# Performance work log

Hardware: AMD Instinct MI355X
Metric: run time of the kernel (lower is better)

## Reference

```python
import jax, jax.numpy as jnp
import numpy as np
import math

L = 2; B = 128; CIN = 64; E = 64; H = 8; Wd = 8; NH = 8; MEM = 40
HD = E // NH; HW = H * Wd; THD = HD * HW  # 512
MASK_B = 3.0; NEG = -1e9; EPS = 1e-5


def _conv(x, w, b):
    y = jax.lax.conv_general_dilated(x, w, (1, 1), 'SAME',
                                     dimension_numbers=('NCHW', 'OIHW', 'NCHW'))
    return y + b[None, :, None, None]


def setup_inputs() -> dict:
    key = jax.random.key(0)
    ks = jax.random.split(key, 12)
    f = jax.random.normal
    return {
        'x': f(ks[0], (B, CIN, H, Wd), jnp.float32),
        'h0': f(ks[1], (L, B, E, H, Wd), jnp.float32),
        'c0': f(ks[2], (L, B, E, H, Wd), jnp.float32),
        'k0': f(ks[3], (L, B, NH, MEM, THD), jnp.float32),
        'v0': f(ks[4], (L, B, NH, MEM, THD), jnp.float32),
        'src_mask': jax.random.randint(ks[5], (B, MEM), 0, 2).astype(bool),
        'notdone': jnp.ones((B,), bool),
        'main_w': f(ks[6], (L, 5 * E, CIN + 2 * E, 3, 3), jnp.float32) * 0.05,
        'main_b': jnp.zeros((L, 5 * E), jnp.float32),
        'proj_w': f(ks[7], (L, 3 * E, CIN + E, 3, 3), jnp.float32) * 0.05,
        'proj_b': jnp.zeros((L, 3 * E), jnp.float32),
        'out_w': f(ks[8], (L, E, E, 3, 3), jnp.float32) * 0.05,
        'out_b': jnp.zeros((L, E), jnp.float32),
        'ln_w': jnp.ones((L, E, H, Wd), jnp.float32),
        'ln_b': jnp.zeros((L, E, H, Wd), jnp.float32),
        'pos_w': f(ks[9], (L, MEM, HW * E), jnp.float32) * 0.05,
        'pos_b': f(ks[10], (L, MEM, NH), jnp.float32) * 0.05,
    }


def reference(x, h0, c0, k0, v0, src_mask, notdone,
              main_w, main_b, proj_w, proj_b, out_w, out_b,
              ln_w, ln_b, pos_w, pos_b):
    nd = notdone.astype(x.dtype)[:, None, None, None]
    # rolling attention mask: reset finished episodes, shift left, open last slot
    m = src_mask | (~notdone)[:, None]
    m = jnp.concatenate([m[:, 1:], jnp.zeros((B, 1), bool)], axis=1)
    bias = jnp.where(m, NEG, 0.0).astype(x.dtype)        # (B, MEM)
    bias = bias.at[:, -1].set(MASK_B)
    out = h0[L - 1] * nd
    for n in range(L):
        inp = jnp.concatenate([x, out], axis=1)          # (B, CIN+E, H, W)
        h_cur = h0[n] * nd
        c_cur = c0[n] * nd
        gates = _conv(jnp.concatenate([inp, h_cur], axis=1), main_w[n], main_b[n])
        cc_i, cc_f, cc_o, cc_g, cc_a = jnp.split(gates, 5, axis=1)
        i = jax.nn.sigmoid(cc_i)
        fg = jax.nn.sigmoid(cc_f)
        o = jax.nn.sigmoid(cc_o)
        g = jnp.tanh(cc_g)
        a = jax.nn.sigmoid(cc_a)
        c_next = fg * c_cur + i * g
        # attention over rolling memory (mem_n slots of flattened spatial features)
        kqv = _conv(inp, proj_w[n], proj_b[n]).reshape(B, NH, 3 * HD, HW)
        k = kqv[:, :, :HD].reshape(B, NH, THD)
        q = kqv[:, :, HD:2 * HD].reshape(B, NH, THD) / math.sqrt(THD)
        v = kqv[:, :, 2 * HD:].reshape(B, NH, THD)
        pw = pos_w[n].reshape(MEM, NH, THD).transpose(1, 0, 2)  # (NH, MEM, THD)
        k_cat = jnp.concatenate([k0[n][:, :, 1:], k[:, :, None, :]], axis=2) + pw[None]
        v_cat = jnp.concatenate([v0[n][:, :, 1:], v[:, :, None, :]], axis=2)
        scores = (jnp.einsum('bnd,bnmd->bnm', q, k_cat)
                  + bias[:, None, :] + pos_b[n].T[None])
        attn_w = jax.nn.softmax(scores, axis=-1)
        attn = jnp.einsum('bnm,bnmd->bnd', attn_w, v_cat).reshape(B, E, H, Wd)
        ao = _conv(attn, out_w[n], out_b[n]) + inp[:, :E]
        mu = ao.mean(axis=(1, 2, 3), keepdims=True)
        var = ((ao - mu) ** 2).mean(axis=(1, 2, 3), keepdims=True)
        ao = (ao - mu) * jax.lax.rsqrt(var + EPS) * ln_w[n][None] + ln_b[n][None]
        c_next = c_next + a * jnp.tanh(ao)
        out = o * jnp.tanh(c_next)
    return out
```

## Files before the change

### kernel.cpp

```cpp
#include <hip/hip_runtime.h>
#include <hip/hip_bf16.h>

typedef __hip_bfloat16 bf16;
typedef unsigned short u16;
typedef __attribute__((ext_vector_type(8))) short short8;
typedef __attribute__((ext_vector_type(4))) float f32x4;

#define Bb   128
#define MEMm 40

__device__ __forceinline__ float LD(const void* p, size_t i, int f32) {
    return f32 ? ((const float*)p)[i] : __bfloat162float(((const bf16*)p)[i]);
}
__device__ __forceinline__ float S2F(short s) {
    u16 u = (u16)s;
    return __bfloat162float(*(bf16*)&u);
}
__device__ __forceinline__ int LDB(const void* p, int i, int isbyte) {
    return isbyte ? (int)((const unsigned char*)p)[i] : ((const int*)p)[i];
}
__device__ __forceinline__ void SPLIT(float v, u16& hi, u16& lo) {
    bf16 h = __float2bfloat16(v);
    float r = v - __bfloat162float(h);
    bf16 l = __float2bfloat16(r);
    hi = *(u16*)&h; lo = *(u16*)&l;
}

__global__ void detect_kernel(const void* __restrict__ x,
                              const void* __restrict__ src_mask,
                              const void* __restrict__ notdone,
                              int* __restrict__ flags) {
    __shared__ int s[3];
    const int t = threadIdx.x;
    if (t < 3) s[t] = 0;
    __syncthreads();
    const bf16* xb = (const bf16*)x;
    int bad = 0;
    for (int i = t; i < 4096; i += 256) {
        float v = __bfloat162float(xb[2 * i]);
        if (!(fabsf(v) < 1e4f)) bad = 1;
    }
    if (bad) atomicOr(&s[0], 1);
    int mb = 0;
    const unsigned* mi = (const unsigned*)src_mask;
    for (int i = t; i < 1280; i += 256) if (mi[i] > 1u) mb = 1;
    if (mb) atomicOr(&s[1], 1);
    int nb = 0;
    const unsigned* ni = (const unsigned*)notdone;
    for (int i = t; i < 32; i += 256) if (ni[i] > 1u) nb = 1;
    if (nb) atomicOr(&s[2], 1);
    __syncthreads();
    if (t < 3) flags[t] = s[t];
}

__global__ void setup_kernel(const void* __restrict__ src_mask,
                             const void* __restrict__ notdone,
                             const void* __restrict__ h0,
                             const void* __restrict__ mw,
                             const void* __restrict__ pw,
                             const void* __restrict__ ow,
                             const int* __restrict__ flags,
                             float* __restrict__ biasb,
                             float* __restrict__ outb, size_t hoff,
                             u16* __restrict__ whi, u16* __restrict__ wlo) {
    const int bid = blockIdx.x, t = threadIdx.x;
    const int isf32 = flags[0], mbyte = flags[1], ndbyte = flags[2];
    if (bid < 20) {
        int idx = bid * 256 + t;
        if (idx >= Bb * MEMm) return;
        int b = idx / MEMm, m = idx - b * MEMm;
        float v;
        if (m == MEMm - 1) v = 3.0f;
        else {
            bool masked = (LDB(src_mask, b * MEMm + m + 1, mbyte) != 0) ||
                          (LDB(notdone, b, ndbyte) == 0);
            v = masked ? -1e9f : 0.f;
        }
        biasb[idx] = v;
    } else if (bid < 276) {
        int idx = (bid - 20) * 256 + t;
        int b = idx >> 9;
        float nd = (LDB(notdone, b, ndbyte) != 0) ? 1.f : 0.f;
        size_t e = (size_t)idx * 8;
        float v[8];
        if (isf32) {
            const float* hp = (const float*)h0 + hoff + e;
            f32x4 a = *(const f32x4*)hp, c = *(const f32x4*)(hp + 4);
#pragma unroll
            for (int j = 0; j < 4; ++j) { v[j] = a[j]; v[4 + j] = c[j]; }
        } else {
            short8 s = *(const short8*)((const bf16*)h0 + hoff + e);
#pragma unroll
            for (int j = 0; j < 8; ++j) v[j] = S2F(s[j]);
        }
#pragma unroll
        for (int j = 0; j < 8; ++j) outb[e + j] = v[j] * nd;
    } else {
        int gi = (bid - 276) * 256 + t;
        if (gi >= 1622016) return;
        int layer = (gi >= 811008) ? 1 : 0;
        int i = gi - layer * 811008;
        float v;
        if (i < 552960) {
            int tap = i / 61440, r = i - tap * 61440, co = r / 192, ci = r - co * 192;
            v = LD(mw, (size_t)layer * 552960 + ((size_t)co * 192 + ci) * 9 + tap, isf32);
        } else if (i < 774144) {
            int j = i - 552960;
            int tap = j / 24576, r = j - tap * 24576, co = r / 128, ci = r - co * 128;
            v = LD(pw, (size_t)layer * 221184 + ((size_t)co * 128 + ci) * 9 + tap, isf32);
        } else {
            int j = i - 774144;
            int tap = j / 4096, r = j - tap * 4096, co = r / 64, ci = r - co * 64;
            v = LD(ow, (size_t)layer * 36864 + ((size_t)co * 64 + ci) * 9 + tap, isf32);
        }
        u16 h, l; SPLIT(v, h, l);
        whi[gi] = h; wlo[gi] = l;
    }
}

struct ConvArgs {
    const void *x; const float *prev_out; const void *h0; const void *notdone;
    const u16 *WhiA, *WloA, *WhiB, *WloB;
    const void *biasA, *biasB;
    float *OutA, *OutB;
    long long boffA, boffB;
    size_t hoff;
    int KciA, KciB, CoutA, CoutB, ntA, NT, NMB;
};

__global__ __launch_bounds__(256) void conv_mfma_kernel(ConvArgs g,
                                                        const int* __restrict__ flags) {
    __shared__ __align__(16) u16 Alds[2][2][2600];
    __shared__ __align__(16) u16 Wlds[2][2][2560];
    const int t = threadIdx.x, w = t >> 6, lane = t & 63;
    const int bpair = w >> 1, half = w & 1;
    const int bx = blockIdx.x;
    const int mblk = bx % g.NMB, nt = bx / g.NMB;
    const bool isA = (nt < g.ntA);
    const u16* Whi = isA ? g.WhiA : g.WhiB;
    const u16* Wlo = isA ? g.WloA : g.WloB;
    const int Kci  = isA ? g.KciA : g.KciB;
    const int CoutT= isA ? g.CoutA : g.CoutB;
    float* Out     = isA ? g.OutA : g.OutB;
    const void* bias = isA ? g.biasA : g.biasB;
    const long long boff = isA ? g.boffA : g.boffB;
    const int n0 = (isA ? nt : nt - g.ntA) * 64;
    const int b = mblk * 2 + bpair;
    const int NITER = (Kci >> 5) * 9;
    const int isf32 = flags[0];
    const float nd = (LDB(g.notdone, b, flags[2]) != 0) ? 1.f : 0.f;

    if (half == 0 && lane < 40) { Alds[bpair][0][2560 + lane] = 0; Alds[bpair][1][2560 + lane] = 0; }

    f32x4 acc[4][2];
#pragma unroll
    for (int i = 0; i < 4; ++i)
#pragma unroll
        for (int j = 0; j < 2; ++j) { f32x4 z = {0.f, 0.f, 0.f, 0.f}; acc[i][j] = z; }

    const int co_l = t >> 2, jj = t & 3;
    uint4 hv, lv;
    auto issueW = [&](int it) {
        int kc = it / 9, tap = it - kc * 9;
        size_t o = ((size_t)(tap * CoutT + n0 + co_l)) * Kci + kc * 32 + jj * 8;
        hv = *(const uint4*)(Whi + o);
        lv = *(const uint4*)(Wlo + o);
    };

    issueW(0);
    for (int it = 0; it < NITER; ++it) {
        const int kc = it / 9, tap = it - kc * 9;
        const int par = it & 1;
        *(uint4*)&Wlds[par][0][co_l * 40 + jj * 8] = hv;
        *(uint4*)&Wlds[par][1][co_l * 40 + jj * 8] = lv;
        __syncthreads();
        if (it + 1 < NITER) issueW(it + 1);
        if (tap == 0) {
            const int px = lane;
            const int c0i = half * 16;
            const int cbase = kc * 32;
            short8 hA, hB, lA, lB;
#pragma unroll
            for (int cl2 = 0; cl2 < 16; ++cl2) {
                int c = cbase + c0i + cl2;
                float v;
                if (c < 64) {
                    size_t o = (size_t)b * 4096 + (size_t)c * 64 + px;
                    v = isf32 ? ((const float*)g.x)[o] : S2F(((const short*)g.x)[o]);
                } else if (c < 128) {
                    v = g.prev_out[(size_t)b * 4096 + (size_t)(c - 64) * 64 + px];
                } else {
                    size_t o = g.hoff + (size_t)b * 4096 + (size_t)(c - 128) * 64 + px;
                    v = (isf32 ? ((const float*)g.h0)[o] : S2F(((const short*)g.h0)[o])) * nd;
                }
                u16 hh, ll; SPLIT(v, hh, ll);
                if (cl2 < 8) { hA[cl2] = (short)hh; lA[cl2] = (short)ll; }
                else         { hB[cl2 - 8] = (short)hh; lB[cl2 - 8] = (short)ll; }
            }
            *(short8*)&Alds[bpair][0][px * 40 + c0i]     = hA;
            *(short8*)&Alds[bpair][0][px * 40 + c0i + 8] = hB;
            *(short8*)&Alds[bpair][1][px * 40 + c0i]     = lA;
            *(short8*)&Alds[bpair][1][px * 40 + c0i + 8] = lB;
            __syncthreads();
        }
        const int dy = tap / 3 - 1, dx = tap % 3 - 1;
        const int q8 = (lane >> 4) * 8;
        const int ml = lane & 15;
        short8 aH[4], aL[4];
#pragma unroll
        for (int mt = 0; mt < 4; ++mt) {
            int px = mt * 16 + ml;
            int yy = (px >> 3) + dy, xx = (px & 7) + dx;
            int row = ((unsigned)yy < 8u && (unsigned)xx < 8u) ? yy * 8 + xx : 64;
            int o = row * 40 + q8;
            aH[mt] = *(const short8*)&Alds[bpair][0][o];
            aL[mt] = *(const short8*)&Alds[bpair][1][o];
        }
#pragma unroll
        for (int nn = 0; nn < 2; ++nn) {
            int o = (half * 32 + nn * 16 + ml) * 40 + q8;
            short8 bH = *(const short8*)&Wlds[par][0][o];
            short8 bL = *(const short8*)&Wlds[par][1][o];
#pragma unroll
            for (int mt = 0; mt < 4; ++mt) {
                acc[mt][nn] = __builtin_amdgcn_mfma_f32_16x16x32_bf16(aH[mt], bH, acc[mt][nn], 0, 0, 0);
                acc[mt][nn] = __builtin_amdgcn_mfma_f32_16x16x32_bf16(aH[mt], bL, acc[mt][nn], 0, 0, 0);
                acc[mt][nn] = __builtin_amdgcn_mfma_f32_16x16x32_bf16(aL[mt], bH, acc[mt][nn], 0, 0, 0);
            }
        }
    }
    const int q = lane >> 4, ml = lane & 15;
#pragma unroll
    for (int nn = 0; nn < 2; ++nn) {
        int co = n0 + half * 32 + nn * 16 + ml;
        float bv = LD(bias, (size_t)boff + co, isf32);
#pragma unroll
        for (int mt = 0; mt < 4; ++mt) {
            f32x4 v = acc[mt][nn];
            v[0] += bv; v[1] += bv; v[2] += bv; v[3] += bv;
            *(f32x4*)&Out[((size_t)b * CoutT + co) * 64 + mt * 16 + q * 4] = v;
        }
    }
}

__global__ __launch_bounds__(256) void attn_kernel(
    const float* __restrict__ kqv,
    const void* __restrict__ k0,
    const void* __restrict__ v0,
    const void* __restrict__ pw,
    const void* __restrict__ pb,
    const float* __restrict__ biasb,
    const int* __restrict__ flags,
    u16* __restrict__ ahi, u16* __restrict__ alo,
    size_t kvoff, size_t pwoff, size_t pboff) {
    __shared__ float qv[512], kl[512], vl[512], sc[40], wexp[40];
    __shared__ float accbuf[4][512];
    const int t = threadIdx.x;
    const int isf32 = flags[0];
    const int b = blockIdx.x >> 3, h = blockIdx.x & 7;
    const size_t kqb = (size_t)b * 192 * 64;
    for (int d = t; d < 512; d += 256) {
        int hd = d >> 6, ss = d & 63;
        qv[d] = kqv[kqb + (h * 24 + 8 + hd) * 64 + ss] * 0.044194173824159216f;
        kl[d] = kqv[kqb + (h * 24 + 0 + hd) * 64 + ss];
        vl[d] = kqv[kqb + (h * 24 + 16 + hd) * 64 + ss];
    }
    __syncthreads();
    const int wid = t >> 6, lane = t & 63;
    const int d0 = lane * 8;
    const size_t kvbase = kvoff + ((size_t)(b * 8 + h)) * (size_t)(40 * 512);

    float q8[8];
#pragma unroll
    for (int j = 0; j < 8; ++j) q8[j] = qv[d0 + j];

    for (int m = wid; m < 40; m += 4) {
        float kc[8];
        if (m < 39) {
            if (isf32) {
                const float* kp = (const float*)k0 + kvbase + (size_t)(m + 1) * 512 + d0;
                f32x4 a = *(const f32x4*)kp, c = *(const f32x4*)(kp + 4);
#pragma unroll
                for (int j = 0; j < 4; ++j) { kc[j] = a[j]; kc[4 + j] = c[j]; }
            } else {
                short8 s = *(const short8*)((const bf16*)k0 + kvbase + (size_t)(m + 1) * 512 + d0);
#pragma unroll
                for (int j = 0; j < 8; ++j) kc[j] = S2F(s[j]);
            }
        } else {
#pragma unroll
            for (int j = 0; j < 8; ++j) kc[j] = kl[d0 + j];
        }
        if (isf32) {
            const float* pp = (const float*)pw + pwoff + (size_t)m * 4096 + h * 512 + d0;
            f32x4 a = *(const f32x4*)pp, c = *(const f32x4*)(pp + 4);
#pragma unroll
            for (int j = 0; j < 4; ++j) { kc[j] += a[j]; kc[4 + j] += c[j]; }
        } else {
            short8 s = *(const short8*)((const bf16*)pw + pwoff + (size_t)m * 4096 + h * 512 + d0);
#pragma unroll
            for (int j = 0; j < 8; ++j) kc[j] += S2F(s[j]);
        }
        float p = 0.f;
#pragma unroll
        for (int j = 0; j < 8; ++j) p += q8[j] * kc[j];
#pragma unroll
        for (int off = 32; off > 0; off >>= 1) p += __shfl_down(p, off, 64);
        if (lane == 0)
            sc[m] = p + biasb[b * 40 + m] + LD(pb, pboff + m * 8 + h, isf32);
    }
    __syncthreads();

    float mx = -1e30f;
    for (int m = 0; m < 40; ++m) mx = fmaxf(mx, sc[m]);
    if (t < 40) wexp[t] = __expf(sc[t] - mx);
    __syncthreads();
    float sum = 0.f;
    for (int m = 0; m < 40; ++m) sum += wexp[m];
    float rs = 1.f / sum;

    float acc8[8];
#pragma unroll
    for (int j = 0; j < 8; ++j) acc8[j] = 0.f;
    for (int m = wid; m < 40; m += 4) {
        float wgt = wexp[m];
        if (m < 39) {
            if (isf32) {
                const float* vp = (const float*)v0 + kvbase + (size_t)(m + 1) * 512 + d0;
                f32x4 a = *(const f32x4*)vp, c = *(const f32x4*)(vp + 4);
#pragma unroll
                for (int j = 0; j < 4; ++j) { acc8[j] += wgt * a[j]; acc8[4 + j] += wgt * c[j]; }
            } else {
                short8 s = *(const short8*)((const bf16*)v0 + kvbase + (size_t)(m + 1) * 512 + d0);
#pragma unroll
                for (int j = 0; j < 8; ++j) acc8[j] += wgt * S2F(s[j]);
            }
        } else {
#pragma unroll
            for (int j = 0; j < 8; ++j) acc8[j] += wgt * vl[d0 + j];
        }
    }
#pragma unroll
    for (int j = 0; j < 8; ++j) accbuf[wid][d0 + j] = acc8[j];
    __syncthreads();

    for (int d = t; d < 512; d += 256) {
        float acc = (accbuf[0][d] + accbuf[1][d]) + (accbuf[2][d] + accbuf[3][d]);
        acc *= rs;
        int ch = h * 8 + (d >> 6), px = d & 63;
        u16 hh, ll; SPLIT(acc, hh, ll);
        size_t o = (size_t)b * 4096 + px * 64 + ch;
        ahi[o] = hh; alo[o] = ll;
    }
}

__global__ __launch_bounds__(256) void tail_kernel(
    const u16* __restrict__ ahi, const u16* __restrict__ alo,
    const u16* __restrict__ whi, const u16* __restrict__ wlo,
    const void* __restrict__ outb_bias,
    const void* __restrict__ x,
    const float* __restrict__ gates,
    const void* __restrict__ c0,
    const void* __restrict__ notdone,
    const void* __restrict__ lnw, const void* __restrict__ lnb,
    const int* __restrict__ flags,
    float* __restrict__ out_buf, void* __restrict__ dout, int write_out,
    long long boff, size_t coff, size_t lnoff) {
    __shared__ __align__(16) u16 Ald[2][2][2600];
    __shared__ __align__(16) u16 Wl[2][2][2560];
    __shared__ float red[8], stats[2];
    const int t = threadIdx.x, w = t >> 6, lane = t & 63;
    const int b = blockIdx.x;
    const int isf32 = flags[0], ndbyte = flags[2];

    {
        int px = t >> 2, ci16 = (t & 3) * 16;
        int chunk = ci16 >> 5, cl = ci16 & 31;
        size_t o = ((size_t)b * 64 + px) * 64 + ci16;
        *(uint4*)&Ald[chunk][0][px * 40 + cl]     = *(const uint4*)(ahi + o);
        *(uint4*)&Ald[chunk][0][px * 40 + cl + 8] = *(const uint4*)(ahi + o + 8);
        *(uint4*)&Ald[chunk][1][px * 40 + cl]     = *(const uint4*)(alo + o);
        *(uint4*)&Ald[chunk][1][px * 40 + cl + 8] = *(const uint4*)(alo + o + 8);
        if (t < 160) { int ch = t / 80, hl = (t / 40) & 1, i = t % 40;
                       Ald[ch][hl][2560 + i] = 0; }
    }

    const int co_l = t >> 2, jj = t & 3;
    uint4 hv, lv;
    auto issueW = [&](int it) {
        int kc = it / 9, tap = it - kc * 9;
        size_t o = ((size_t)(tap * 64 + co_l)) * 64 + kc * 32 + jj * 8;
        hv = *(const uint4*)(whi + o);
        lv = *(const uint4*)(wlo + o);
    };

    f32x4 acc[4];
#pragma unroll
    for (int i = 0; i < 4; ++i) { f32x4 z = {0.f, 0.f, 0.f, 0.f}; acc[i] = z; }

    issueW(0);
    for (int it = 0; it < 18; ++it) {
        const int kc = it / 9, tap = it - kc * 9;
        const int par = it & 1;
        *(uint4*)&Wl[par][0][co_l * 40 + jj * 8] = hv;
        *(uint4*)&Wl[par][1][co_l * 40 + jj * 8] = lv;
        __syncthreads();
        if (it + 1 < 18) issueW(it + 1);
        const int dy = tap / 3 - 1, dx = tap % 3 - 1;
        const int q8 = (lane >> 4) * 8;
        const int ml = lane & 15;
        short8 aH[4], aL[4];
#pragma unroll
        for (int mt = 0; mt < 4; ++mt) {
            int px = mt * 16 + ml;
            int yy = (px >> 3) + dy, xx = (px & 7) + dx;
            int row = ((unsigned)yy < 8u && (unsigned)xx < 8u) ? yy * 8 + xx : 64;
            int o = row * 40 + q8;
            aH[mt] = *(const short8*)&Ald[kc][0][o];
            aL[mt] = *(const short8*)&Ald[kc][1][o];
        }
        int o = (w * 16 + ml) * 40 + q8;
        short8 bH = *(const short8*)&Wl[par][0][o];
        short8 bL = *(const short8*)&Wl[par][1][o];
#pragma unroll
        for (int mt = 0; mt < 4; ++mt) {
            acc[mt] = __builtin_amdgcn_mfma_f32_16x16x32_bf16(aH[mt], bH, acc[mt], 0, 0, 0);
            acc[mt] = __builtin_amdgcn_mfma_f32_16x16x32_bf16(aH[mt], bL, acc[mt], 0, 0, 0);
            acc[mt] = __builtin_amdgcn_mfma_f32_16x16x32_bf16(aL[mt], bH, acc[mt], 0, 0, 0);
        }
    }

    const int q = lane >> 4, ml = lane & 15;
    const int co = w * 16 + ml;
    const size_t base = (size_t)b * 4096;
    float bv = LD(outb_bias, (size_t)boff + co, isf32);
    float vals[16];
    float sum = 0.f, sumsq = 0.f;
#pragma unroll
    for (int mt = 0; mt < 4; ++mt) {
        int px0 = mt * 16 + q * 4;
#pragma unroll
        for (int r = 0; r < 4; ++r) {
            float xv = LD(x, base + (size_t)co * 64 + px0 + r, isf32);
            float val = acc[mt][r] + bv + xv;
            vals[mt * 4 + r] = val; sum += val; sumsq += val * val;
        }
    }
#pragma unroll
    for (int off = 32; off > 0; off >>= 1) {
        sum   += __shfl_down(sum, off, 64);
        sumsq += __shfl_down(sumsq, off, 64);
    }
    if (lane == 0) { red[w] = sum; red[4 + w] = sumsq; }
    __syncthreads();
    if (t == 0) {
        float ts = red[0] + red[1] + red[2] + red[3];
        float tq = red[4] + red[5] + red[6] + red[7];
        float mu = ts * (1.f / 4096.f);
        float var = tq * (1.f / 4096.f) - mu * mu;
        stats[0] = mu; stats[1] = rsqrtf(fmaxf(var, 0.f) + 1e-5f);
    }
    __syncthreads();
    const float mu = stats[0], rstd = stats[1];
    const float nd = (LDB(notdone, b, ndbyte) != 0) ? 1.f : 0.f;
    const size_t gbase = (size_t)b * 320 * 64;
#pragma unroll
    for (int mt = 0; mt < 4; ++mt) {
        int px0 = mt * 16 + q * 4;
        size_t i0 = (size_t)co * 64 + px0;
        f32x4 gi4 = *(const f32x4*)&gates[gbase + (size_t)(co      ) * 64 + px0];
        f32x4 gf4 = *(const f32x4*)&gates[gbase + (size_t)(co +  64) * 64 + px0];
        f32x4 go4 = *(const f32x4*)&gates[gbase + (size_t)(co + 128) * 64 + px0];
        f32x4 gg4 = *(const f32x4*)&gates[gbase + (size_t)(co + 192) * 64 + px0];
        f32x4 ga4 = *(const f32x4*)&gates[gbase + (size_t)(co + 256) * 64 + px0];
        f32x4 ov;
#pragma unroll
        for (int r = 0; r < 4; ++r) {
            size_t i = i0 + r;
            float aon = (vals[mt * 4 + r] - mu) * rstd * LD(lnw, lnoff + i, isf32)
                        + LD(lnb, lnoff + i, isf32);
            float gi = 1.f / (1.f + __expf(-gi4[r]));
            float gf = 1.f / (1.f + __expf(-gf4[r]));
            float go = 1.f / (1.f + __expf(-go4[r]));
            float gg = tanhf(gg4[r]);
            float ga = 1.f / (1.f + __expf(-ga4[r]));
            float cc = LD(c0, coff + base + i, isf32) * nd;
            float cn = gf * cc + gi * gg + ga * tanhf(aon);
            float o  = go * tanhf(cn);
            ov[r] = o;
            if (write_out) {
                if (isf32) ((float*)dout)[base + i] = o;
                else       ((bf16*)dout)[base + i] = __float2bfloat16(o);
            }
        }
        *(f32x4*)&out_buf[base + i0] = ov;
    }
}

extern "C" void kernel_launch(void* const* d_in, const int* in_sizes, int n_in,
                              void* d_out, int out_size, void* d_ws, size_t ws_size,
                              hipStream_t stream) {
    const void* x      = d_in[0];
    const void* h0     = d_in[1];
    const void* c0     = d_in[2];
    const void* k0     = d_in[3];
    const void* v0     = d_in[4];
    const void* src_mask = d_in[5];
    const void* notdone  = d_in[6];
    const void* main_w = d_in[7];
    const void* main_b = d_in[8];
    const void* proj_w = d_in[9];
    const void* proj_b = d_in[10];
    const void* out_w  = d_in[11];
    const void* out_b  = d_in[12];
    const void* ln_w   = d_in[13];
    const void* ln_b   = d_in[14];
    const void* pos_w  = d_in[15];
    const void* pos_b  = d_in[16];

    float* wsf = (float*)d_ws;
    int*   flags    = (int*)d_ws;
    float* bias_buf = wsf + 8;
    float* out_buf  = wsf + 8192;
    float* gates_buf= wsf + 532480;
    float* kqv_buf  = wsf + 3153920;
    u16* attn_hi    = (u16*)(wsf + 4726784);
    u16* attn_lo    = (u16*)(wsf + 4988928);
    u16* wr_hi      = (u16*)(wsf + 5251072);
    u16* wr_lo      = (u16*)(wsf + 6062080);

    detect_kernel<<<1, 256, 0, stream>>>(x, src_mask, notdone, flags);
    setup_kernel<<<6612, 256, 0, stream>>>(src_mask, notdone, h0,
                                           main_w, proj_w, out_w, flags,
                                           bias_buf, out_buf, (size_t)524288,
                                           wr_hi, wr_lo);
    for (int n = 0; n < 2; ++n) {
        const size_t wb = (size_t)n * 811008;
        ConvArgs ga;
        ga.x = x; ga.prev_out = out_buf; ga.h0 = h0; ga.notdone = notdone;
        ga.hoff = (size_t)n * 524288;
        ga.WhiA = wr_hi + wb;          ga.WloA = wr_lo + wb;          ga.KciA = 192; ga.CoutA = 320;
        ga.WhiB = wr_hi + wb + 552960; ga.WloB = wr_lo + wb + 552960; ga.KciB = 128; ga.CoutB = 192;
        ga.biasA = main_b; ga.boffA = (long long)n * 320; ga.OutA = gates_buf;
        ga.biasB = proj_b; ga.boffB = (long long)n * 192; ga.OutB = kqv_buf;
        ga.ntA = 5; ga.NT = 8; ga.NMB = 64;
        conv_mfma_kernel<<<512, 256, 0, stream>>>(ga, flags);

        attn_kernel<<<1024, 256, 0, stream>>>(
            kqv_buf, k0, v0, pos_w, pos_b, bias_buf, flags, attn_hi, attn_lo,
            (size_t)n * 20971520, (size_t)n * 163840, (size_t)n * 320);

        tail_kernel<<<128, 256, 0, stream>>>(
            attn_hi, attn_lo, wr_hi + wb + 774144, wr_lo + wb + 774144,
            out_b, x, gates_buf, c0, notdone, ln_w, ln_b, flags,
            out_buf, d_out, (n == 1) ? 1 : 0,
            (long long)n * 64, (size_t)n * 524288, (size_t)n * 4096);
    }
}
```

Before: 572.5 us.

## Fuse all stages into one cooperative persistent kernel with grid syncs

```diff
diff --git a/kernel.cpp b/kernel.cpp
--- a/kernel.cpp
+++ b/kernel.cpp
@@ -1,5 +1,8 @@
 #include <hip/hip_runtime.h>
 #include <hip/hip_bf16.h>
+#include <hip/hip_cooperative_groups.h>
+
+namespace cg = cooperative_groups;
 
 typedef __hip_bfloat16 bf16;
 typedef unsigned short u16;
@@ -25,6 +28,470 @@
     bf16 l = __float2bfloat16(r);
     hi = *(u16*)&h; lo = *(u16*)&l;
 }
+
+struct __align__(16) ShConv { u16 Alds[2][2][2600]; u16 Wlds[2][2][2560]; };
+struct __align__(16) ShAttn { float qv[512], kl[512], vl[512], sc[40], wexp[40];
+                              float accbuf[4][512]; };
+struct __align__(16) ShTail { u16 Ald[2][2][2600]; u16 Wl[2][2][2560];
+                              float red[8]; float stats[2]; };
+union __align__(16) Sh { int det[3]; ShConv conv; ShAttn attn; ShTail tail; };
+
+struct FusedArgs {
+    const void *x, *h0, *c0, *k0, *v0, *src_mask, *notdone;
+    const void *main_w, *main_b, *proj_w, *proj_b, *out_w, *out_b;
+    const void *ln_w, *ln_b, *pos_w, *pos_b;
+    float *bias_buf, *out_buf, *gates_buf, *kqv_buf;
+    u16 *attn_hi, *attn_lo, *wr_hi, *wr_lo;
+    void *dout;
+};
+
+__global__ __launch_bounds__(256, 2) void fused_kernel(FusedArgs a) {
+    __shared__ Sh sh;
+    cg::grid_group grid = cg::this_grid();
+    const int t = threadIdx.x, bx = blockIdx.x;
+
+    int isf32, mbyte, ndbyte;
+    {
+        if (t < 3) sh.det[t] = 0;
+        __syncthreads();
+        const bf16* xb = (const bf16*)a.x;
+        int bad = 0;
+        for (int i = t; i < 4096; i += 256) {
+            float v = __bfloat162float(xb[2 * i]);
+            if (!(fabsf(v) < 1e4f)) bad = 1;
+        }
+        if (bad) atomicOr(&sh.det[0], 1);
+        int mb = 0;
+        const unsigned* mi = (const unsigned*)a.src_mask;
+        for (int i = t; i < 1280; i += 256) if (mi[i] > 1u) mb = 1;
+        if (mb) atomicOr(&sh.det[1], 1);
+        int nb = 0;
+        const unsigned* ni = (const unsigned*)a.notdone;
+        for (int i = t; i < 32; i += 256) if (ni[i] > 1u) nb = 1;
+        if (nb) atomicOr(&sh.det[2], 1);
+        __syncthreads();
+        isf32 = sh.det[0]; mbyte = sh.det[1]; ndbyte = sh.det[2];
+        __syncthreads();
+    }
+
+    for (int u = bx; u < 6612; u += 512) {
+        if (u < 20) {
+            int idx = u * 256 + t;
+            if (idx < Bb * MEMm) {
+                int b = idx / MEMm, m = idx - b * MEMm;
+                float v;
+                if (m == MEMm - 1) v = 3.0f;
+                else {
+                    bool masked = (LDB(a.src_mask, b * MEMm + m + 1, mbyte) != 0) ||
+                                  (LDB(a.notdone, b, ndbyte) == 0);
+                    v = masked ? -1e9f : 0.f;
+                }
+                a.bias_buf[idx] = v;
+            }
+        } else if (u < 276) {
+            int idx = (u - 20) * 256 + t;
+            int b = idx >> 9;
+            float nd = (LDB(a.notdone, b, ndbyte) != 0) ? 1.f : 0.f;
+            size_t e = (size_t)idx * 8;
+            float v[8];
+            if (isf32) {
+                const float* hp = (const float*)a.h0 + 524288 + e;
+                f32x4 p0 = *(const f32x4*)hp, p1 = *(const f32x4*)(hp + 4);
+#pragma unroll
+                for (int j = 0; j < 4; ++j) { v[j] = p0[j]; v[4 + j] = p1[j]; }
+            } else {
+                short8 s = *(const short8*)((const bf16*)a.h0 + 524288 + e);
+#pragma unroll
+                for (int j = 0; j < 8; ++j) v[j] = S2F(s[j]);
+            }
+#pragma unroll
+            for (int j = 0; j < 8; ++j) a.out_buf[e + j] = v[j] * nd;
+        } else {
+            int gi = (u - 276) * 256 + t;
+            if (gi < 1622016) {
+                int layer = (gi >= 811008) ? 1 : 0;
+                int i = gi - layer * 811008;
+                float v;
+                if (i < 552960) {
+                    int tap = i / 61440, r = i - tap * 61440, co = r / 192, ci = r - co * 192;
+                    v = LD(a.main_w, (size_t)layer * 552960 + ((size_t)co * 192 + ci) * 9 + tap, isf32);
+                } else if (i < 774144) {
+                    int j = i - 552960;
+                    int tap = j / 24576, r = j - tap * 24576, co = r / 128, ci = r - co * 128;
+                    v = LD(a.proj_w, (size_t)layer * 221184 + ((size_t)co * 128 + ci) * 9 + tap, isf32);
+                } else {
+                    int j = i - 774144;
+                    int tap = j / 4096, r = j - tap * 4096, co = r / 64, ci = r - co * 64;
+                    v = LD(a.out_w, (size_t)layer * 36864 + ((size_t)co * 64 + ci) * 9 + tap, isf32);
+                }
+                u16 h, l; SPLIT(v, h, l);
+                a.wr_hi[gi] = h; a.wr_lo[gi] = l;
+            }
+        }
+    }
+    grid.sync();
+
+#pragma unroll 1
+    for (int n = 0; n < 2; ++n) {
+        const size_t wb = (size_t)n * 811008;
+        const size_t hoff = (size_t)n * 524288;
+
+        {
+            auto& Alds = sh.conv.Alds;
+            auto& Wlds = sh.conv.Wlds;
+            const int w = t >> 6, lane = t & 63;
+            const int bpair = w >> 1, half = w & 1;
+            const int mblk = bx & 63, nt = bx >> 6;
+            const bool isA = (nt < 5);
+            const u16* Whi = a.wr_hi + wb + (isA ? 0 : 552960);
+            const u16* Wlo = a.wr_lo + wb + (isA ? 0 : 552960);
+            const int Kci  = isA ? 192 : 128;
+            const int CoutT= isA ? 320 : 192;
+            float* Out     = isA ? a.gates_buf : a.kqv_buf;
+            const void* bias = isA ? a.main_b : a.proj_b;
+            const long long boff = isA ? (long long)n * 320 : (long long)n * 192;
+            const int n0 = (isA ? nt : nt - 5) * 64;
+            const int b = mblk * 2 + bpair;
+            const int NITER = (Kci >> 5) * 9;
+            const float nd = (LDB(a.notdone, b, ndbyte) != 0) ? 1.f : 0.f;
+
+            if (half == 0 && lane < 40) { Alds[bpair][0][2560 + lane] = 0; Alds[bpair][1][2560 + lane] = 0; }
+
+            f32x4 acc[4][2];
+#pragma unroll
+            for (int i = 0; i < 4; ++i)
+#pragma unroll
+                for (int j = 0; j < 2; ++j) { f32x4 z = {0.f, 0.f, 0.f, 0.f}; acc[i][j] = z; }
+
+            const int co_l = t >> 2, jj = t & 3;
+            uint4 hv, lv;
+            auto issueW = [&](int it) {
+                int kc = it / 9, tap = it - kc * 9;
+                size_t o = ((size_t)(tap * CoutT + n0 + co_l)) * Kci + kc * 32 + jj * 8;
+                hv = *(const uint4*)(Whi + o);
+                lv = *(const uint4*)(Wlo + o);
+            };
+
+            issueW(0);
+            for (int it = 0; it < NITER; ++it) {
+                const int kc = it / 9, tap = it - kc * 9;
+                const int par = it & 1;
+                *(uint4*)&Wlds[par][0][co_l * 40 + jj * 8] = hv;
+                *(uint4*)&Wlds[par][1][co_l * 40 + jj * 8] = lv;
+                __syncthreads();
+                if (it + 1 < NITER) issueW(it + 1);
+                if (tap == 0) {
+                    const int px = lane;
+                    const int c0i = half * 16;
+                    const int cbase = kc * 32;
+                    short8 hA, hB, lA, lB;
+#pragma unroll
+                    for (int cl2 = 0; cl2 < 16; ++cl2) {
+                        int c = cbase + c0i + cl2;
+                        float v;
+                        if (c < 64) {
+                            size_t o = (size_t)b * 4096 + (size_t)c * 64 + px;
+                            v = isf32 ? ((const float*)a.x)[o] : S2F(((const short*)a.x)[o]);
+                        } else if (c < 128) {
+                            v = a.out_buf[(size_t)b * 4096 + (size_t)(c - 64) * 64 + px];
+                        } else {
+                            size_t o = hoff + (size_t)b * 4096 + (size_t)(c - 128) * 64 + px;
+                            v = (isf32 ? ((const float*)a.h0)[o] : S2F(((const short*)a.h0)[o])) * nd;
+                        }
+                        u16 hh, ll; SPLIT(v, hh, ll);
+                        if (cl2 < 8) { hA[cl2] = (short)hh; lA[cl2] = (short)ll; }
+                        else         { hB[cl2 - 8] = (short)hh; lB[cl2 - 8] = (short)ll; }
+                    }
+                    *(short8*)&Alds[bpair][0][px * 40 + c0i]     = hA;
+                    *(short8*)&Alds[bpair][0][px * 40 + c0i + 8] = hB;
+                    *(short8*)&Alds[bpair][1][px * 40 + c0i]     = lA;
+                    *(short8*)&Alds[bpair][1][px * 40 + c0i + 8] = lB;
+                    __syncthreads();
+                }
+                const int dy = tap / 3 - 1, dx = tap % 3 - 1;
+                const int q8 = (lane >> 4) * 8;
+                const int ml = lane & 15;
+                short8 aH[4], aL[4];
+#pragma unroll
+                for (int mt = 0; mt < 4; ++mt) {
+                    int px = mt * 16 + ml;
+                    int yy = (px >> 3) + dy, xx = (px & 7) + dx;
+                    int row = ((unsigned)yy < 8u && (unsigned)xx < 8u) ? yy * 8 + xx : 64;
+                    int o = row * 40 + q8;
+                    aH[mt] = *(const short8*)&Alds[bpair][0][o];
+                    aL[mt] = *(const short8*)&Alds[bpair][1][o];
+                }
+#pragma unroll
+                for (int nn = 0; nn < 2; ++nn) {
+                    int o = (half * 32 + nn * 16 + ml) * 40 + q8;
+                    short8 bH = *(const short8*)&Wlds[par][0][o];
+                    short8 bL = *(const short8*)&Wlds[par][1][o];
+#pragma unroll
+                    for (int mt = 0; mt < 4; ++mt) {
+                        acc[mt][nn] = __builtin_amdgcn_mfma_f32_16x16x32_bf16(aH[mt], bH, acc[mt][nn], 0, 0, 0);
+                        acc[mt][nn] = __builtin_amdgcn_mfma_f32_16x16x32_bf16(aH[mt], bL, acc[mt][nn], 0, 0, 0);
+                        acc[mt][nn] = __builtin_amdgcn_mfma_f32_16x16x32_bf16(aL[mt], bH, acc[mt][nn], 0, 0, 0);
+                    }
+                }
+            }
+            const int q = lane >> 4, ml = lane & 15;
+#pragma unroll
+            for (int nn = 0; nn < 2; ++nn) {
+                int co = n0 + half * 32 + nn * 16 + ml;
+                float bv = LD(bias, (size_t)boff + co, isf32);
+#pragma unroll
+                for (int mt = 0; mt < 4; ++mt) {
+                    f32x4 v = acc[mt][nn];
+                    v[0] += bv; v[1] += bv; v[2] += bv; v[3] += bv;
+                    *(f32x4*)&Out[((size_t)b * CoutT + co) * 64 + mt * 16 + q * 4] = v;
+                }
+            }
+        }
+        grid.sync();
+
+        for (int u = bx; u < 1024; u += 512) {
+            float* qv = sh.attn.qv; float* kl = sh.attn.kl; float* vl = sh.attn.vl;
+            float* sc = sh.attn.sc; float* wexp = sh.attn.wexp;
+            auto& accbuf = sh.attn.accbuf;
+            const int b = u >> 3, h = u & 7;
+            const size_t kqb = (size_t)b * 192 * 64;
+            for (int d = t; d < 512; d += 256) {
+                int hd = d >> 6, ss = d & 63;
+                qv[d] = a.kqv_buf[kqb + (h * 24 + 8 + hd) * 64 + ss] * 0.044194173824159216f;
+                kl[d] = a.kqv_buf[kqb + (h * 24 + 0 + hd) * 64 + ss];
+                vl[d] = a.kqv_buf[kqb + (h * 24 + 16 + hd) * 64 + ss];
+            }
+            __syncthreads();
+            const int wid = t >> 6, lane = t & 63;
+            const int d0 = lane * 8;
+            const size_t kvbase = (size_t)n * 20971520 + ((size_t)(b * 8 + h)) * (size_t)(40 * 512);
+            const size_t pwoff = (size_t)n * 163840, pboff = (size_t)n * 320;
+
+            float q8[8];
+#pragma unroll
+            for (int j = 0; j < 8; ++j) q8[j] = qv[d0 + j];
+
+            for (int m = wid; m < 40; m += 4) {
+                float kc[8];
+                if (m < 39) {
+                    if (isf32) {
+                        const float* kp = (const float*)a.k0 + kvbase + (size_t)(m + 1) * 512 + d0;
+                        f32x4 p0 = *(const f32x4*)kp, p1 = *(const f32x4*)(kp + 4);
+#pragma unroll
+                        for (int j = 0; j < 4; ++j) { kc[j] = p0[j]; kc[4 + j] = p1[j]; }
+                    } else {
+                        short8 s = *(const short8*)((const bf16*)a.k0 + kvbase + (size_t)(m + 1) * 512 + d0);
+#pragma unroll
+                        for (int j = 0; j < 8; ++j) kc[j] = S2F(s[j]);
+                    }
+                } else {
+#pragma unroll
+                    for (int j = 0; j < 8; ++j) kc[j] = kl[d0 + j];
+                }
+                if (isf32) {
+                    const float* pp = (const float*)a.pos_w + pwoff + (size_t)m * 4096 + h * 512 + d0;
+                    f32x4 p0 = *(const f32x4*)pp, p1 = *(const f32x4*)(pp + 4);
+#pragma unroll
+                    for (int j = 0; j < 4; ++j) { kc[j] += p0[j]; kc[4 + j] += p1[j]; }
+                } else {
+                    short8 s = *(const short8*)((const bf16*)a.pos_w + pwoff + (size_t)m * 4096 + h * 512 + d0);
+#pragma unroll
+                    for (int j = 0; j < 8; ++j) kc[j] += S2F(s[j]);
+                }
+                float p = 0.f;
+#pragma unroll
+                for (int j = 0; j < 8; ++j) p += q8[j] * kc[j];
+#pragma unroll
+                for (int off = 32; off > 0; off >>= 1) p += __shfl_down(p, off, 64);
+                if (lane == 0)
+                    sc[m] = p + a.bias_buf[b * 40 + m] + LD(a.pos_b, pboff + m * 8 + h, isf32);
+            }
+            __syncthreads();
+
+            float mx = -1e30f;
+            for (int m = 0; m < 40; ++m) mx = fmaxf(mx, sc[m]);
+            if (t < 40) wexp[t] = __expf(sc[t] - mx);
+            __syncthreads();
+            float sum = 0.f;
+            for (int m = 0; m < 40; ++m) sum += wexp[m];
+            float rs = 1.f / sum;
+
+            float acc8[8];
+#pragma unroll
+            for (int j = 0; j < 8; ++j) acc8[j] = 0.f;
+            for (int m = wid; m < 40; m += 4) {
+                float wgt = wexp[m];
+                if (m < 39) {
+                    if (isf32) {
+                        const float* vp = (const float*)a.v0 + kvbase + (size_t)(m + 1) * 512 + d0;
+                        f32x4 p0 = *(const f32x4*)vp, p1 = *(const f32x4*)(vp + 4);
+#pragma unroll
+                        for (int j = 0; j < 4; ++j) { acc8[j] += wgt * p0[j]; acc8[4 + j] += wgt * p1[j]; }
+                    } else {
+                        short8 s = *(const short8*)((const bf16*)a.v0 + kvbase + (size_t)(m + 1) * 512 + d0);
+#pragma unroll
+                        for (int j = 0; j < 8; ++j) acc8[j] += wgt * S2F(s[j]);
+                    }
+                } else {
+#pragma unroll
+                    for (int j = 0; j < 8; ++j) acc8[j] += wgt * vl[d0 + j];
+                }
+            }
+#pragma unroll
+            for (int j = 0; j < 8; ++j) accbuf[wid][d0 + j] = acc8[j];
+            __syncthreads();
+
+            for (int d = t; d < 512; d += 256) {
+                float acc = (accbuf[0][d] + accbuf[1][d]) + (accbuf[2][d] + accbuf[3][d]);
+                acc *= rs;
+                int ch = h * 8 + (d >> 6), px = d & 63;
+                u16 hh, ll; SPLIT(acc, hh, ll);
+                size_t o = (size_t)b * 4096 + px * 64 + ch;
+                a.attn_hi[o] = hh; a.attn_lo[o] = ll;
+            }
+            __syncthreads();
+        }
+        grid.sync();
+
+        if (bx < 128) {
+            auto& Ald = sh.tail.Ald;
+            auto& Wl  = sh.tail.Wl;
+            float* red = sh.tail.red; float* stats = sh.tail.stats;
+            const int w = t >> 6, lane = t & 63;
+            const int b = bx;
+            const u16* whi = a.wr_hi + wb + 774144;
+            const u16* wlo = a.wr_lo + wb + 774144;
+            const int write_out = (n == 1) ? 1 : 0;
+            const long long boff = (long long)n * 64;
+            const size_t coff = (size_t)n * 524288, lnoff = (size_t)n * 4096;
+
+            {
+                int px = t >> 2, ci16 = (t & 3) * 16;
+                int chunk = ci16 >> 5, cl = ci16 & 31;
+                size_t o = ((size_t)b * 64 + px) * 64 + ci16;
+                *(uint4*)&Ald[chunk][0][px * 40 + cl]     = *(const uint4*)(a.attn_hi + o);
+                *(uint4*)&Ald[chunk][0][px * 40 + cl + 8] = *(const uint4*)(a.attn_hi + o + 8);
+                *(uint4*)&Ald[chunk][1][px * 40 + cl]     = *(const uint4*)(a.attn_lo + o);
+                *(uint4*)&Ald[chunk][1][px * 40 + cl + 8] = *(const uint4*)(a.attn_lo + o + 8);
+                if (t < 160) { int ch = t / 80, hl = (t / 40) & 1, i = t % 40;
+                               Ald[ch][hl][2560 + i] = 0; }
+            }
+
+            const int co_l = t >> 2, jj = t & 3;
+            uint4 hv, lv;
+            auto issueW = [&](int it) {
+                int kc = it / 9, tap = it - kc * 9;
+                size_t o = ((size_t)(tap * 64 + co_l)) * 64 + kc * 32 + jj * 8;
+                hv = *(const uint4*)(whi + o);
+                lv = *(const uint4*)(wlo + o);
+            };
+
+            f32x4 acc[4];
+#pragma unroll
+            for (int i = 0; i < 4; ++i) { f32x4 z = {0.f, 0.f, 0.f, 0.f}; acc[i] = z; }
+
+            issueW(0);
+            for (int it = 0; it < 18; ++it) {
+                const int kc = it / 9, tap = it - kc * 9;
+                const int par = it & 1;
+                *(uint4*)&Wl[par][0][co_l * 40 + jj * 8] = hv;
+                *(uint4*)&Wl[par][1][co_l * 40 + jj * 8] = lv;
+                __syncthreads();
+                if (it + 1 < 18) issueW(it + 1);
+                const int dy = tap / 3 - 1, dx = tap % 3 - 1;
+                const int q8 = (lane >> 4) * 8;
+                const int ml = lane & 15;
+                short8 aH[4], aL[4];
+#pragma unroll
+                for (int mt = 0; mt < 4; ++mt) {
+                    int px = mt * 16 + ml;
+                    int yy = (px >> 3) + dy, xx = (px & 7) + dx;
+                    int row = ((unsigned)yy < 8u && (unsigned)xx < 8u) ? yy * 8 + xx : 64;
+                    int o = row * 40 + q8;
+                    aH[mt] = *(const short8*)&Ald[kc][0][o];
+                    aL[mt] = *(const short8*)&Ald[kc][1][o];
+                }
+                int o = (w * 16 + ml) * 40 + q8;
+                short8 bH = *(const short8*)&Wl[par][0][o];
+                short8 bL = *(const short8*)&Wl[par][1][o];
+#pragma unroll
+                for (int mt = 0; mt < 4; ++mt) {
+                    acc[mt] = __builtin_amdgcn_mfma_f32_16x16x32_bf16(aH[mt], bH, acc[mt], 0, 0, 0);
+                    acc[mt] = __builtin_amdgcn_mfma_f32_16x16x32_bf16(aH[mt], bL, acc[mt], 0, 0, 0);
+                    acc[mt] = __builtin_amdgcn_mfma_f32_16x16x32_bf16(aL[mt], bH, acc[mt], 0, 0, 0);
+                }
+            }
+
+            const int q = lane >> 4, ml = lane & 15;
+            const int co = w * 16 + ml;
+            const size_t base = (size_t)b * 4096;
+            float bv = LD(a.out_b, (size_t)boff + co, isf32);
+            float vals[16];
+            float sum = 0.f, sumsq = 0.f;
+#pragma unroll
+            for (int mt = 0; mt < 4; ++mt) {
+                int px0 = mt * 16 + q * 4;
+#pragma unroll
+                for (int r = 0; r < 4; ++r) {
+                    float xv = LD(a.x, base + (size_t)co * 64 + px0 + r, isf32);
+                    float val = acc[mt][r] + bv + xv;
+                    vals[mt * 4 + r] = val; sum += val; sumsq += val * val;
+                }
+            }
+#pragma unroll
+            for (int off = 32; off > 0; off >>= 1) {
+                sum   += __shfl_down(sum, off, 64);
+                sumsq += __shfl_down(sumsq, off, 64);
+            }
+            if (lane == 0) { red[w] = sum; red[4 + w] = sumsq; }
+            __syncthreads();
+            if (t == 0) {
+                float ts = red[0] + red[1] + red[2] + red[3];
+                float tq = red[4] + red[5] + red[6] + red[7];
+                float mu = ts * (1.f / 4096.f);
+                float var = tq * (1.f / 4096.f) - mu * mu;
+                stats[0] = mu; stats[1] = rsqrtf(fmaxf(var, 0.f) + 1e-5f);
+            }
+            __syncthreads();
+            const float mu = stats[0], rstd = stats[1];
+            const float nd = (LDB(a.notdone, b, ndbyte) != 0) ? 1.f : 0.f;
+            const size_t gbase = (size_t)b * 320 * 64;
+#pragma unroll
+            for (int mt = 0; mt < 4; ++mt) {
+                int px0 = mt * 16 + q * 4;
+                size_t i0 = (size_t)co * 64 + px0;
+                f32x4 gi4 = *(const f32x4*)&a.gates_buf[gbase + (size_t)(co      ) * 64 + px0];
+                f32x4 gf4 = *(const f32x4*)&a.gates_buf[gbase + (size_t)(co +  64) * 64 + px0];
+                f32x4 go4 = *(const f32x4*)&a.gates_buf[gbase + (size_t)(co + 128) * 64 + px0];
+                f32x4 gg4 = *(const f32x4*)&a.gates_buf[gbase + (size_t)(co + 192) * 64 + px0];
+                f32x4 ga4 = *(const f32x4*)&a.gates_buf[gbase + (size_t)(co + 256) * 64 + px0];
+                f32x4 ov;
+#pragma unroll
+                for (int r = 0; r < 4; ++r) {
+                    size_t i = i0 + r;
+                    float aon = (vals[mt * 4 + r] - mu) * rstd * LD(a.ln_w, lnoff + i, isf32)
+                                + LD(a.ln_b, lnoff + i, isf32);
+                    float gi = 1.f / (1.f + __expf(-gi4[r]));
+                    float gf = 1.f / (1.f + __expf(-gf4[r]));
+                    float go = 1.f / (1.f + __expf(-go4[r]));
+                    float gg = tanhf(gg4[r]);
+                    float ga = 1.f / (1.f + __expf(-ga4[r]));
+                    float cc = LD(a.c0, coff + base + i, isf32) * nd;
+                    float cn = gf * cc + gi * gg + ga * tanhf(aon);
+                    float o  = go * tanhf(cn);
+                    ov[r] = o;
+                    if (write_out) {
+                        if (isf32) ((float*)a.dout)[base + i] = o;
+                        else       ((bf16*)a.dout)[base + i] = __float2bfloat16(o);
+                    }
+                }
+                *(f32x4*)&a.out_buf[base + i0] = ov;
+            }
+        }
+        if (n == 0) grid.sync();
+    }
+}
+
 
 __global__ void detect_kernel(const void* __restrict__ x,
                               const void* __restrict__ src_mask,
@@ -85,9 +552,9 @@
         float v[8];
         if (isf32) {
             const float* hp = (const float*)h0 + hoff + e;
-            f32x4 a = *(const f32x4*)hp, c = *(const f32x4*)(hp + 4);
-#pragma unroll
-            for (int j = 0; j < 4; ++j) { v[j] = a[j]; v[4 + j] = c[j]; }
+            f32x4 p0 = *(const f32x4*)hp, p1 = *(const f32x4*)(hp + 4);
+#pragma unroll
+            for (int j = 0; j < 4; ++j) { v[j] = p0[j]; v[4 + j] = p1[j]; }
         } else {
             short8 s = *(const short8*)((const bf16*)h0 + hoff + e);
 #pragma unroll
@@ -279,9 +746,9 @@
         if (m < 39) {
             if (isf32) {
                 const float* kp = (const float*)k0 + kvbase + (size_t)(m + 1) * 512 + d0;
-                f32x4 a = *(const f32x4*)kp, c = *(const f32x4*)(kp + 4);
-#pragma unroll
-                for (int j = 0; j < 4; ++j) { kc[j] = a[j]; kc[4 + j] = c[j]; }
+                f32x4 p0 = *(const f32x4*)kp, p1 = *(const f32x4*)(kp + 4);
+#pragma unroll
+                for (int j = 0; j < 4; ++j) { kc[j] = p0[j]; kc[4 + j] = p1[j]; }
             } else {
                 short8 s = *(const short8*)((const bf16*)k0 + kvbase + (size_t)(m + 1) * 512 + d0);
 #pragma unroll
@@ -293,9 +760,9 @@
         }
         if (isf32) {
             const float* pp = (const float*)pw + pwoff + (size_t)m * 4096 + h * 512 + d0;
-            f32x4 a = *(const f32x4*)pp, c = *(const f32x4*)(pp + 4);
-#pragma unroll
-            for (int j = 0; j < 4; ++j) { kc[j] += a[j]; kc[4 + j] += c[j]; }
+            f32x4 p0 = *(const f32x4*)pp, p1 = *(const f32x4*)(pp + 4);
+#pragma unroll
+            for (int j = 0; j < 4; ++j) { kc[j] += p0[j]; kc[4 + j] += p1[j]; }
         } else {
             short8 s = *(const short8*)((const bf16*)pw + pwoff + (size_t)m * 4096 + h * 512 + d0);
 #pragma unroll
@@ -327,9 +794,9 @@
         if (m < 39) {
             if (isf32) {
                 const float* vp = (const float*)v0 + kvbase + (size_t)(m + 1) * 512 + d0;
-                f32x4 a = *(const f32x4*)vp, c = *(const f32x4*)(vp + 4);
-#pragma unroll
-                for (int j = 0; j < 4; ++j) { acc8[j] += wgt * a[j]; acc8[4 + j] += wgt * c[j]; }
+                f32x4 p0 = *(const f32x4*)vp, p1 = *(const f32x4*)(vp + 4);
+#pragma unroll
+                for (int j = 0; j < 4; ++j) { acc8[j] += wgt * p0[j]; acc8[4 + j] += wgt * p1[j]; }
             } else {
                 short8 s = *(const short8*)((const bf16*)v0 + kvbase + (size_t)(m + 1) * 512 + d0);
 #pragma unroll
@@ -529,6 +996,26 @@
     u16* wr_hi      = (u16*)(wsf + 5251072);
     u16* wr_lo      = (u16*)(wsf + 6062080);
 
+    FusedArgs fa;
+    fa.x = x; fa.h0 = h0; fa.c0 = c0; fa.k0 = k0; fa.v0 = v0;
+    fa.src_mask = src_mask; fa.notdone = notdone;
+    fa.main_w = main_w; fa.main_b = main_b; fa.proj_w = proj_w; fa.proj_b = proj_b;
+    fa.out_w = out_w; fa.out_b = out_b; fa.ln_w = ln_w; fa.ln_b = ln_b;
+    fa.pos_w = pos_w; fa.pos_b = pos_b;
+    fa.bias_buf = bias_buf; fa.out_buf = out_buf; fa.gates_buf = gates_buf;
+    fa.kqv_buf = kqv_buf; fa.attn_hi = attn_hi; fa.attn_lo = attn_lo;
+    fa.wr_hi = wr_hi; fa.wr_lo = wr_lo; fa.dout = d_out;
+
+    int maxB = 0;
+    hipError_t occ = hipOccupancyMaxActiveBlocksPerMultiprocessor(&maxB, fused_kernel, 256, 0);
+    if (occ == hipSuccess && maxB >= 2) {
+        void* kargs[] = { (void*)&fa };
+        hipError_t e = hipLaunchCooperativeKernel(fused_kernel, dim3(512), dim3(256),
+                                                  kargs, 0u, stream);
+        if (e == hipSuccess) return;
+        (void)hipGetLastError();
+    }
+
     detect_kernel<<<1, 256, 0, stream>>>(x, src_mask, notdone, flags);
     setup_kernel<<<6612, 256, 0, stream>>>(src_mask, notdone, h0,
                                            main_w, proj_w, out_w, flags,
```

Measured after the change: 573.4 us. Within noise of the previous version (+0.2%).
